# Performance work log

Measured on AMD Instinct MI355X. Metric: run time of the kernel, lower is better.

Reference implementation:

```python
import jax, jax.numpy as jnp
import numpy as np


def _dct_last(x):
    """Unnormalized DCT-II along the last axis via the FFT reorder+twiddle trick:
    v[n] = x[2n], v[N-1-n] = x[2n+1];  y[k] = Re( exp(-i*pi*k/(2N)) * FFT(v)[k] )
    => y[k] = sum_n x[n] * cos(pi*(2n+1)*k/(2N))
    This mirrors DREAMPlace's expk (twiddle) formulation.
    """
    N = x.shape[-1]
    v = jnp.concatenate([x[..., ::2], x[..., 1::2][..., ::-1]], axis=-1)
    V = jnp.fft.fft(v)
    k = jnp.arange(N)
    expk = jnp.exp(-1j * jnp.pi * k.astype(x.dtype) / (2.0 * N))
    return jnp.real(V * expk).astype(x.dtype)


def _dct2(x):
    # DCT-II along last axis, then along second-to-last axis (separable 2D DCT).
    y = _dct_last(x)
    y = _dct_last(jnp.swapaxes(y, -1, -2))
    return jnp.swapaxes(y, -1, -2)


def setup_inputs() -> dict:
    key = jax.random.key(0)
    x = jax.random.normal(key, (8, 2048, 2048), dtype=jnp.float32)
    return {"x": x}


def reference(x):
    return _dct2(x)
```

## Files before the change

### kernel.cpp

```cpp
#include <hip/hip_runtime.h>
#include <hip/hip_bf16.h>
#include <hip/hip_fp16.h>


typedef _Float16 half8 __attribute__((ext_vector_type(8)));
typedef float f32x4 __attribute__((ext_vector_type(4)));
typedef unsigned int uint32;

constexpr int TILE_E = 256 * 32;

__device__ __forceinline__ unsigned short f2h_bits(float f) {
  _Float16 h = (_Float16)f;
  return __builtin_bit_cast(unsigned short, h);
}
__device__ __forceinline__ uint32 pk2(float a, float b) {
  return f2h_bits(a) | ((uint32)f2h_bits(b) << 16);
}

__device__ __forceinline__ void gload_lds16(const unsigned short* g, unsigned short* l) {
  __builtin_amdgcn_global_load_lds((const __attribute__((address_space(1))) void*)g,
                                   (__attribute__((address_space(3))) void*)l,
                                   16, 0, 0);
}

#define CFENCE asm volatile("" ::: "memory")

__device__ __forceinline__ int swz_idx(int r, int cbyte) {
  int b = (r >> 1) * 128 + ((((r & 1) << 6) | cbyte) ^ (((r >> 1) & 7) << 4));
  return b >> 1;
}

__device__ __forceinline__ void stage_tile(const unsigned short* __restrict__ G,
                                           int rowbase, int k0, int ld,
                                           unsigned short* lds, int wave, int lane) {
#pragma unroll
  for (int c = 0; c < 2; ++c) {
    const int p = c * 64 + wave * 8 + (lane >> 3);
    const int v = (lane & 7) ^ ((lane >> 3) & 7);
    const int r = 2 * p + (v >> 2);
    const int kslot = v & 3;
    const unsigned short* src = G + (size_t)(rowbase + r) * ld + (k0 + kslot * 8);
    unsigned short* dst = lds + (c * 64 + wave * 8) * 64;
    gload_lds16(src, dst);
  }
}

__global__ __launch_bounds__(512) void cvt_fold22(const float* __restrict__ x,
                                                  unsigned short* __restrict__ Xff) {
  __shared__ float Y[4][2048];
  const int blk = blockIdx.x;
  const int b = blk >> 9;
  const int v = blk & 511;
  const int j = threadIdx.x;
  const float* base = x + (size_t)b * 4194304;
  const float* r0 = base + (size_t)v * 2048;
  const float* r1 = base + (size_t)(2047 - v) * 2048;
  const float* r2 = base + (size_t)(1023 - v) * 2048;
  const float* r3 = base + (size_t)(1024 + v) * 2048;

  {
    const int c = 4 * j;
    float4 a = *(const float4*)(r0 + c);
    float4 bb = *(const float4*)(r1 + c);
    float4 cc = *(const float4*)(r2 + c);
    float4 dd = *(const float4*)(r3 + c);
    float4 sp, sm, d0, d1;
    sp.x = (a.x + bb.x) + (cc.x + dd.x); sm.x = (a.x + bb.x) - (cc.x + dd.x);
    sp.y = (a.y + bb.y) + (cc.y + dd.y); sm.y = (a.y + bb.y) - (cc.y + dd.y);
    sp.z = (a.z + bb.z) + (cc.z + dd.z); sm.z = (a.z + bb.z) - (cc.z + dd.z);
    sp.w = (a.w + bb.w) + (cc.w + dd.w); sm.w = (a.w + bb.w) - (cc.w + dd.w);
    d0.x = a.x - bb.x; d1.x = cc.x - dd.x;
    d0.y = a.y - bb.y; d1.y = cc.y - dd.y;
    d0.z = a.z - bb.z; d1.z = cc.z - dd.z;
    d0.w = a.w - bb.w; d1.w = cc.w - dd.w;
    *(float4*)&Y[0][c] = sp;
    *(float4*)&Y[1][c] = sm;
    *(float4*)&Y[2][c] = d0;
    *(float4*)&Y[3][c] = d1;
  }
  __syncthreads();

  unsigned short* orow[4] = {
      Xff + ((size_t)b * 2048 + v) * 2048,
      Xff + ((size_t)b * 2048 + 512 + v) * 2048,
      Xff + ((size_t)b * 2048 + 1024 + v) * 2048,
      Xff + ((size_t)b * 2048 + 2047 - v) * 2048};
  const int c0 = 4 * j;
  int pA, pD, pB, pC, rng;
  if (j < 128) { rng = 0; pA = 4 * j; pD = 2044 - 4 * j; pB = 1020 - 4 * j; pC = 1024 + 4 * j; }
  else if (j < 256) { rng = 1; pA = 4 * j - 512; pD = 2556 - 4 * j; pB = 1532 - 4 * j; pC = 512 + 4 * j; }
  else { rng = 2; pA = 4 * j - 1024; pD = 3068 - 4 * j; pB = 0; pC = 0; }

#pragma unroll
  for (int t = 0; t < 4; ++t) {
    float val[4];
    float4 av = *(const float4*)&Y[t][pA];
    float4 dv = *(const float4*)&Y[t][pD];
    const float* A = (const float*)&av;
    const float* Dq = (const float*)&dv;
    if (rng == 2) {
#pragma unroll
      for (int e = 0; e < 4; ++e) val[e] = A[e] - Dq[3 - e];
    } else {
      float4 bv = *(const float4*)&Y[t][pB];
      float4 cv = *(const float4*)&Y[t][pC];
      const float* Bq = (const float*)&bv;
      const float* Cq = (const float*)&cv;
#pragma unroll
      for (int e = 0; e < 4; ++e) {
        float P = A[e] + Dq[3 - e];
        float M = Bq[3 - e] + Cq[e];
        val[e] = rng == 0 ? P + M : P - M;
      }
    }
    *(uint2*)(orow[t] + c0) = make_uint2(pk2(val[0], val[1]), pk2(val[2], val[3]));
  }
}

__global__ __launch_bounds__(256) void gen_cos3(unsigned short* __restrict__ C4k,
                                                unsigned short* __restrict__ C2h,
                                                unsigned short* __restrict__ C4h) {
  int idx = blockIdx.x * 256 + threadIdx.x;
  const float s = 7.6699039394282061e-4f;
  if (idx < 1048576) {
    int k = idx >> 10, n = idx & 1023;
    int t = ((2 * n + 1) * (2 * k + 1)) & 8191;
    C4k[idx] = f2h_bits(cosf((float)t * s));
  } else if (idx < 1310720) {
    int i2 = idx - 1048576;
    int k = i2 >> 9, n = i2 & 511;
    int t = ((2 * n + 1) * 4 * k) & 8191;
    C2h[i2] = f2h_bits(cosf((float)t * s));
  } else {
    int i2 = idx - 1310720;
    int k = i2 >> 9, n = i2 & 511;
    int t = ((2 * n + 1) * (4 * k + 2)) & 8191;
    C4h[i2] = f2h_bits(cosf((float)t * s));
  }
}

template <int MODE, int SPLIT>
__global__ __launch_bounds__(512) void dct_gemm(
    const unsigned short* __restrict__ M0, const unsigned short* __restrict__ M1,
    const unsigned short* __restrict__ D, void* __restrict__ outp) {
  constexpr int K = SPLIT ? 512 : 1024;
  constexpr int NT = K / 32;
  __shared__ unsigned short As[4 * TILE_E];
  __shared__ unsigned short Bs[4 * TILE_E];

  const int tid = threadIdx.x;
  const int lane = tid & 63;
  const int wave = tid >> 6;
  const int wr = wave >> 2;
  const int wc = wave & 3;

  int lin, f, bmx, bnx, z;
  if (MODE == 0) {
    lin = blockIdx.y * 4 + blockIdx.x;
    f = (lin & 7) * 32 + (lin >> 3);
    bnx = f & 3;
    bmx = f >> 2;
    z = 0;
  } else {
    lin = (blockIdx.z * 4 + blockIdx.y) * 8 + blockIdx.x;
    f = (lin & 7) * 32 + (lin >> 3);
    bnx = f & 7;
    bmx = (f >> 3) & 3;
    z = f >> 5;
  }

  const unsigned short* Ag;
  const unsigned short* Bg;
  int lda, ldb, arow, brow, cls;
  if (MODE == 0) {
    cls = SPLIT ? (bnx >> 1) : 0;
    Ag = D + (SPLIT ? cls * 512 : 1024);
    lda = 2048;
    arow = bmx * 256;
    Bg = SPLIT ? (cls ? M1 : M0) : M0;
    ldb = K;
    brow = (SPLIT ? (bnx & 1) : bnx) * 256;
  } else {
    cls = SPLIT ? (bmx >> 1) : 0;
    Ag = SPLIT ? (cls ? M1 : M0) : M0;
    lda = K;
    arow = (SPLIT ? (bmx & 1) : bmx) * 256;
    Bg = D + (size_t)z * 4194304u + (SPLIT ? cls * 512 : 1024);
    ldb = 2048;
    brow = bnx * 256;
  }

  const int frc = lane & 15;
  const int cb = (lane >> 4) << 4;

  f32x4 acc[8][4] = {};

  stage_tile(Ag, arow, 0, lda, &As[0], wave, lane);
  stage_tile(Bg, brow, 0, ldb, &Bs[0], wave, lane);
  stage_tile(Ag, arow, 32, lda, &As[TILE_E], wave, lane);
  stage_tile(Bg, brow, 32, ldb, &Bs[TILE_E], wave, lane);
  asm volatile("s_waitcnt vmcnt(4)" ::: "memory");
  CFENCE; __builtin_amdgcn_s_barrier(); CFENCE;

  for (int t = 0; t < NT; ++t) {
    const unsigned short* at = &As[(t & 3) * TILE_E];
    const unsigned short* bt = &Bs[(t & 3) * TILE_E];
    half8 af[4], bf[4];

#pragma unroll
    for (int m = 0; m < 4; ++m)
      af[m] = *(const half8*)&at[swz_idx(wr * 128 + m * 16 + frc, cb)];
#pragma unroll
    for (int n = 0; n < 4; ++n)
      bf[n] = *(const half8*)&bt[swz_idx(wc * 64 + n * 16 + frc, cb)];
    if (t + 2 < NT)
      stage_tile(Ag, arow, (t + 2) * 32, lda, &As[((t + 2) & 3) * TILE_E], wave, lane);
    CFENCE; __builtin_amdgcn_s_barrier(); CFENCE;
    __builtin_amdgcn_s_setprio(1);
#pragma unroll
    for (int m = 0; m < 4; ++m)
#pragma unroll
      for (int n = 0; n < 4; ++n)
        acc[m][n] = __builtin_amdgcn_mfma_f32_16x16x32_f16(af[m], bf[n], acc[m][n], 0, 0, 0);
    __builtin_amdgcn_s_setprio(0);

#pragma unroll
    for (int m = 0; m < 4; ++m)
      af[m] = *(const half8*)&at[swz_idx(wr * 128 + 64 + m * 16 + frc, cb)];
    if (t + 2 < NT)
      stage_tile(Bg, brow, (t + 2) * 32, ldb, &Bs[((t + 2) & 3) * TILE_E], wave, lane);
    if (t < NT - 2)
      asm volatile("s_waitcnt vmcnt(4)" ::: "memory");
    else if (t == NT - 2)
      asm volatile("s_waitcnt vmcnt(0)" ::: "memory");
    CFENCE; __builtin_amdgcn_s_barrier(); CFENCE;
    __builtin_amdgcn_s_setprio(1);
#pragma unroll
    for (int m = 0; m < 4; ++m)
#pragma unroll
      for (int n = 0; n < 4; ++n)
        acc[m + 4][n] =
            __builtin_amdgcn_mfma_f32_16x16x32_f16(af[m], bf[n], acc[m + 4][n], 0, 0, 0);
    __builtin_amdgcn_s_setprio(0);
  }

  if (MODE == 0) {
    unsigned short* U2t = (unsigned short*)outp;
#pragma unroll
    for (int mi = 0; mi < 8; ++mi) {
      const int r = arow + wr * 128 + (mi >> 2) * 64 + (mi & 3) * 16 + (lane >> 4) * 4;
      const int b = r >> 11;
      const int rb = r & 2047;
#pragma unroll
      for (int n = 0; n < 4; ++n) {
        const int ccls = brow + wc * 64 + n * 16 + frc;
        const int ktrue = SPLIT ? (4 * ccls + 2 * cls) : (2 * ccls + 1);
        uint32 lo = f2h_bits(acc[mi][n][0]) | ((uint32)f2h_bits(acc[mi][n][1]) << 16);
        uint32 hi = f2h_bits(acc[mi][n][2]) | ((uint32)f2h_bits(acc[mi][n][3]) << 16);
        *(uint2*)&U2t[(size_t)b * 4194304 + (size_t)ktrue * 2048 + rb] =
            make_uint2(lo, hi);
      }
    }
  } else {
    float* out = (float*)outp + (size_t)z * 4194304;
#pragma unroll
    for (int mi = 0; mi < 8; ++mi) {
      const int p0 = arow + wr * 128 + (mi >> 2) * 64 + (mi & 3) * 16 + (lane >> 4) * 4;
#pragma unroll
      for (int n = 0; n < 4; ++n) {
        const int cg = brow + wc * 64 + n * 16 + frc;
#pragma unroll
        for (int i = 0; i < 4; ++i) {
          const int rtrue = SPLIT ? (4 * (p0 + i) + 2 * cls) : (2 * (p0 + i) + 1);
          out[(size_t)rtrue * 2048 + cg] = acc[mi][n][i];
        }
      }
    }
  }
}

extern "C" void kernel_launch(void* const* d_in, const int* in_sizes, int n_in,
                              void* d_out, int out_size, void* d_ws,
                              size_t ws_size, hipStream_t stream) {
  const float* x = (const float*)d_in[0];
  float* out = (float*)d_out;

  unsigned short* Xff = (unsigned short*)d_ws;
  unsigned short* C4k = Xff + 33554432u;
  unsigned short* C2h = C4k + 1048576u;
  unsigned short* C4h = C2h + 262144u;
  unsigned short* U2t = C4h + 262144u;

  cvt_fold22<<<4096, 512, 0, stream>>>(x, Xff);
  gen_cos3<<<6144, 256, 0, stream>>>(C4k, C2h, C4h);
  dct_gemm<0, 0><<<dim3(4, 64, 1), 512, 0, stream>>>(C4k, C4k, Xff, (void*)U2t);
  dct_gemm<0, 1><<<dim3(4, 64, 1), 512, 0, stream>>>(C2h, C4h, Xff, (void*)U2t);
  dct_gemm<1, 0><<<dim3(8, 4, 8), 512, 0, stream>>>(C4k, C4k, U2t, (void*)out);
  dct_gemm<1, 1><<<dim3(8, 4, 8), 512, 0, stream>>>(C2h, C4h, U2t, (void*)out);
}
```

Measured before the change: 189.4 us.

## Merge cosine generation into fold kernel and fuse split GEMM launches

Cosine-table generation moves into the fold/convert kernel, and the paired full-K and split-K GEMMs for each pass merge into one launch that picks its path per block. This cuts the launch count from six to three and lets the 1024-K and 512-K tiles share the GPU, filling the tail of the shorter pass. In exchange NT and pointers become runtime values, which may cost some unrolling or compiler optimisation, and blocks have uneven work.

```diff
diff --git a/kernel.cpp b/kernel.cpp
--- a/kernel.cpp
+++ b/kernel.cpp
@@ -45,8 +45,10 @@
   }
 }
 
-__global__ __launch_bounds__(512) void cvt_fold22(const float* __restrict__ x,
-                                                  unsigned short* __restrict__ Xff) {
+__global__ __launch_bounds__(512) void cvt_fold22(
+    const float* __restrict__ x, unsigned short* __restrict__ Xff,
+    unsigned short* __restrict__ C4k, unsigned short* __restrict__ C2h,
+    unsigned short* __restrict__ C4h) {
   __shared__ float Y[4][2048];
   const int blk = blockIdx.x;
   const int b = blk >> 9;
@@ -115,12 +117,8 @@
     }
     *(uint2*)(orow[t] + c0) = make_uint2(pk2(val[0], val[1]), pk2(val[2], val[3]));
   }
-}
-
-__global__ __launch_bounds__(256) void gen_cos3(unsigned short* __restrict__ C4k,
-                                                unsigned short* __restrict__ C2h,
-                                                unsigned short* __restrict__ C4h) {
-  int idx = blockIdx.x * 256 + threadIdx.x;
+
+  const int idx = blk * 512 + j;
   const float s = 7.6699039394282061e-4f;
   if (idx < 1048576) {
     int k = idx >> 10, n = idx & 1023;
@@ -131,7 +129,7 @@
     int k = i2 >> 9, n = i2 & 511;
     int t = ((2 * n + 1) * 4 * k) & 8191;
     C2h[i2] = f2h_bits(cosf((float)t * s));
-  } else {
+  } else if (idx < 1572864) {
     int i2 = idx - 1310720;
     int k = i2 >> 9, n = i2 & 511;
     int t = ((2 * n + 1) * (4 * k + 2)) & 8191;
@@ -139,12 +137,11 @@
   }
 }
 
-template <int MODE, int SPLIT>
+template <int MODE>
 __global__ __launch_bounds__(512) void dct_gemm(
-    const unsigned short* __restrict__ M0, const unsigned short* __restrict__ M1,
-    const unsigned short* __restrict__ D, void* __restrict__ outp) {
-  constexpr int K = SPLIT ? 512 : 1024;
-  constexpr int NT = K / 32;
+    const unsigned short* __restrict__ C4k, const unsigned short* __restrict__ C2h,
+    const unsigned short* __restrict__ C4h, const unsigned short* __restrict__ D,
+    void* __restrict__ outp) {
   __shared__ unsigned short As[4 * TILE_E];
   __shared__ unsigned short Bs[4 * TILE_E];
 
@@ -154,40 +151,37 @@
   const int wr = wave >> 2;
   const int wc = wave & 3;
 
-  int lin, f, bmx, bnx, z;
-  if (MODE == 0) {
-    lin = blockIdx.y * 4 + blockIdx.x;
-    f = (lin & 7) * 32 + (lin >> 3);
-    bnx = f & 3;
-    bmx = f >> 2;
-    z = 0;
-  } else {
-    lin = (blockIdx.z * 4 + blockIdx.y) * 8 + blockIdx.x;
-    f = (lin & 7) * 32 + (lin >> 3);
-    bnx = f & 7;
-    bmx = (f >> 3) & 3;
-    z = f >> 5;
-  }
+  int lin;
+  if (MODE == 0)
+    lin = blockIdx.y * 8 + blockIdx.x;
+  else
+    lin = (blockIdx.z * 8 + blockIdx.y) * 8 + blockIdx.x;
+  const int f = (lin & 7) * 64 + (lin >> 3);
+  const int split = f & 1;
+  const int f2 = f >> 1;
+  int bnx, bmx, z;
+  if (MODE == 0) { bnx = f2 & 3; bmx = f2 >> 2; z = 0; }
+  else { bnx = f2 & 7; bmx = (f2 >> 3) & 3; z = f2 >> 5; }
 
   const unsigned short* Ag;
   const unsigned short* Bg;
-  int lda, ldb, arow, brow, cls;
+  int lda, ldb, arow, brow, cls, NT;
   if (MODE == 0) {
-    cls = SPLIT ? (bnx >> 1) : 0;
-    Ag = D + (SPLIT ? cls * 512 : 1024);
-    lda = 2048;
-    arow = bmx * 256;
-    Bg = SPLIT ? (cls ? M1 : M0) : M0;
-    ldb = K;
-    brow = (SPLIT ? (bnx & 1) : bnx) * 256;
+    if (!split) {
+      cls = 0; Ag = D + 1024; lda = 2048; arow = bmx * 256;
+      Bg = C4k; ldb = 1024; brow = bnx * 256; NT = 32;
+    } else {
+      cls = bnx >> 1; Ag = D + cls * 512; lda = 2048; arow = bmx * 256;
+      Bg = cls ? C4h : C2h; ldb = 512; brow = (bnx & 1) * 256; NT = 16;
+    }
   } else {
-    cls = SPLIT ? (bmx >> 1) : 0;
-    Ag = SPLIT ? (cls ? M1 : M0) : M0;
-    lda = K;
-    arow = (SPLIT ? (bmx & 1) : bmx) * 256;
-    Bg = D + (size_t)z * 4194304u + (SPLIT ? cls * 512 : 1024);
-    ldb = 2048;
-    brow = bnx * 256;
+    if (!split) {
+      cls = 0; Ag = C4k; lda = 1024; arow = bmx * 256;
+      Bg = D + (size_t)z * 4194304u + 1024; ldb = 2048; brow = bnx * 256; NT = 32;
+    } else {
+      cls = bmx >> 1; Ag = cls ? C4h : C2h; lda = 512; arow = (bmx & 1) * 256;
+      Bg = D + (size_t)z * 4194304u + cls * 512; ldb = 2048; brow = bnx * 256; NT = 16;
+    }
   }
 
   const int frc = lane & 15;
@@ -254,7 +248,7 @@
 #pragma unroll
       for (int n = 0; n < 4; ++n) {
         const int ccls = brow + wc * 64 + n * 16 + frc;
-        const int ktrue = SPLIT ? (4 * ccls + 2 * cls) : (2 * ccls + 1);
+        const int ktrue = split ? (4 * ccls + 2 * cls) : (2 * ccls + 1);
         uint32 lo = f2h_bits(acc[mi][n][0]) | ((uint32)f2h_bits(acc[mi][n][1]) << 16);
         uint32 hi = f2h_bits(acc[mi][n][2]) | ((uint32)f2h_bits(acc[mi][n][3]) << 16);
         *(uint2*)&U2t[(size_t)b * 4194304 + (size_t)ktrue * 2048 + rb] =
@@ -271,7 +265,7 @@
         const int cg = brow + wc * 64 + n * 16 + frc;
 #pragma unroll
         for (int i = 0; i < 4; ++i) {
-          const int rtrue = SPLIT ? (4 * (p0 + i) + 2 * cls) : (2 * (p0 + i) + 1);
+          const int rtrue = split ? (4 * (p0 + i) + 2 * cls) : (2 * (p0 + i) + 1);
           out[(size_t)rtrue * 2048 + cg] = acc[mi][n][i];
         }
       }
@@ -291,10 +285,7 @@
   unsigned short* C4h = C2h + 262144u;
   unsigned short* U2t = C4h + 262144u;
 
-  cvt_fold22<<<4096, 512, 0, stream>>>(x, Xff);
-  gen_cos3<<<6144, 256, 0, stream>>>(C4k, C2h, C4h);
-  dct_gemm<0, 0><<<dim3(4, 64, 1), 512, 0, stream>>>(C4k, C4k, Xff, (void*)U2t);
-  dct_gemm<0, 1><<<dim3(4, 64, 1), 512, 0, stream>>>(C2h, C4h, Xff, (void*)U2t);
-  dct_gemm<1, 0><<<dim3(8, 4, 8), 512, 0, stream>>>(C4k, C4k, U2t, (void*)out);
-  dct_gemm<1, 1><<<dim3(8, 4, 8), 512, 0, stream>>>(C2h, C4h, U2t, (void*)out);
-}
+  cvt_fold22<<<4096, 512, 0, stream>>>(x, Xff, C4k, C2h, C4h);
+  dct_gemm<0><<<dim3(8, 64, 1), 512, 0, stream>>>(C4k, C2h, C4h, Xff, (void*)U2t);
+  dct_gemm<1><<<dim3(8, 8, 8), 512, 0, stream>>>(C4k, C2h, C4h, U2t, (void*)out);
+}
```

After: 190.0 us. About the same (+0.3%).
